# Kernel tuning notes

Hardware: AMD Instinct MI355X
Metric: run time of the kernel (lower is better)

Reference implementation:

```python
import jax, jax.numpy as jnp
import numpy as np

IN_F = 2048
OUT_F = 2048
N_ROWS = 8192


def _perm(n):
    # t_o(n) is a permutation matrix P with P[i, p(i)] = 1, p(i) = (4i mod n) + (4i // n)
    i = np.arange(n)
    return (4 * i) % n + (4 * i) // n


def _inv(p):
    inv = np.empty_like(p)
    inv[p] = np.arange(len(p))
    return inv

# (P_in^T @ H)[a, :] = H[i, :] where p_in(i) = a  ->  rows indexed by inv(p_in)
_INV_P_IN = _inv(_perm(IN_F))
# (H @ P_out)[:, b] = H[:, j] where p_out(j) = b  ->  cols indexed by inv(p_out)
_INV_P_OUT = _inv(_perm(OUT_F))


def make_quaternion_mul(kernel):
    # kernel: (in//4, out); split along dim 1 into quaternion components
    r, i, j, k = jnp.split(kernel, 4, axis=1)
    r2 = jnp.concatenate([r, -i, -j, -k], axis=1)
    i2 = jnp.concatenate([i, r, -k, j], axis=1)
    j2 = jnp.concatenate([j, k, r, -i], axis=1)
    k2 = jnp.concatenate([k, -j, i, r], axis=1)
    return jnp.concatenate([r2, i2, j2, k2], axis=0)  # (in, out)


def setup_inputs() -> dict:
    key = jax.random.key(0)
    k1, k2, k3 = jax.random.split(key, 3)
    inp = jax.random.normal(k1, (N_ROWS, IN_F), dtype=jnp.float32)
    weight = jax.random.normal(k2, (IN_F // 4, OUT_F), dtype=jnp.float32) * (1.0 / np.sqrt(IN_F // 4))
    bias = jax.random.normal(k3, (OUT_F,), dtype=jnp.float32) * 0.01
    return {"input": inp, "weight": weight, "bias": bias}


def reference(input, weight, bias):
    hamilton = make_quaternion_mul(weight)                 # (in, out)
    # swap=True: hamilton = L^T @ hamilton @ R, both pure permutations
    hamilton = hamilton[_INV_P_IN][:, _INV_P_OUT]
    support = input @ hamilton + bias[None, :]             # (N, out)
    return support
```

## Files before the change

### kernel.cpp

```cpp
#include <hip/hip_runtime.h>
#include <stdint.h>

#define IN_F 2048
#define OUT_F 2048
#define N_ROWS 8192

#define BM 256
#define BN 256
#define BK 32
#define NT (IN_F / BK)
#define TM_TILES (N_ROWS / BM)
#define TN_TILES (OUT_F / BN)
#define NWG (TM_TILES * TN_TILES)
#define TILE_SHORTS (BM * BK)
#define BUF_SHORTS (2 * TILE_SHORTS)

typedef __bf16 bf16x8 __attribute__((ext_vector_type(8)));
typedef float f32x4 __attribute__((ext_vector_type(4)));
typedef unsigned short ushortx8 __attribute__((ext_vector_type(8)));

__device__ __forceinline__ unsigned short f2bf(float f) {
  unsigned u = __builtin_bit_cast(unsigned, f);
  u += 0x7FFFu + ((u >> 16) & 1u);
  return (unsigned short)(u >> 16);
}

__device__ __forceinline__ void async16(void* lds, const void* g) {
  __builtin_amdgcn_global_load_lds(
      (const __attribute__((address_space(1))) void*)(uintptr_t)g,
      (__attribute__((address_space(3))) void*)(uint32_t)(uintptr_t)lds,
      16, 0, 0);
}

__device__ __forceinline__ bf16x8 ld8(const unsigned short* p) {
  return __builtin_bit_cast(bf16x8, *reinterpret_cast<const ushortx8*>(p));
}

__global__ __launch_bounds__(256) void k_prep(const float* __restrict__ A,
                                              unsigned short* __restrict__ AbT,
                                              const float* __restrict__ W,
                                              unsigned short* __restrict__ BtT) {
  const int bid = blockIdx.x;
  if (bid < 8192) {
    const int tile = bid >> 2;
    const int t = ((bid & 3) << 8) + threadIdx.x;
    const int r = t >> 2;
    const int ga = (t & 3) ^ ((r >> 1) & 3);
    const int R = tile >> 6, T = tile & 63;
    const float* src = A + (size_t)(R * 256 + r) * IN_F + T * 32 + ga * 8;
    const float4 v0 = *reinterpret_cast<const float4*>(src);
    const float4 v1 = *reinterpret_cast<const float4*>(src + 4);
    ushortx8 o;
    o[0] = f2bf(v0.x); o[1] = f2bf(v0.y); o[2] = f2bf(v0.z); o[3] = f2bf(v0.w);
    o[4] = f2bf(v1.x); o[5] = f2bf(v1.y); o[6] = f2bf(v1.z); o[7] = f2bf(v1.w);
    *reinterpret_cast<ushortx8*>(AbT + (size_t)tile * 8192 + t * 8) = o;
  } else {
    const int bb = bid - 8192;
    const int tile = bb >> 2;
    const int t = ((bb & 3) << 8) + threadIdx.x;
    const int r = t >> 2;
    const int ga = (t & 3) ^ ((r >> 1) & 3);
    const int Ct = tile >> 6, T = tile & 63;
    const int b = Ct * 256 + r;
    const int c = b & 3, v = b >> 2;
    const int a0 = T * 32 + ga * 8;
    ushortx8 o;
#pragma unroll
    for (int e = 0; e < 8; ++e) {
      const int a = a0 + e;
      const int q = a & 3, u = a >> 2;
      float w = W[(size_t)u * OUT_F + ((q ^ c) << 9) + v];
      if ((0x284E >> ((q << 2) | c)) & 1) w = -w;
      o[e] = f2bf(w);
    }
    *reinterpret_cast<ushortx8*>(BtT + (size_t)tile * 8192 + t * 8) = o;
  }
}

__global__ __launch_bounds__(512, 2) void k_gemm(const unsigned short* __restrict__ AbT,
                                                 const unsigned short* __restrict__ BtT,
                                                 const float* __restrict__ bias,
                                                 float* __restrict__ C) {
  __shared__ __align__(16) unsigned short lds[4 * BUF_SHORTS];

  const int tid = threadIdx.x;
  const int lane = tid & 63;
  const int w = tid >> 6;
  const int wm = w >> 2;
  const int wn = w & 3;
  const int fr = lane & 15;
  const int g = lane >> 4;

  const int wg = blockIdx.x;
  const int swz = (wg & 7) * (NWG >> 3) + (wg >> 3);
  const int tm = swz >> 3;
  const int tn = swz & 7;
  const int row0 = tm * BM, col0 = tn * BN;

  const unsigned short* baseA = AbT + (size_t)tm * 64 * 8192;
  const unsigned short* baseB = BtT + (size_t)tn * 64 * 8192;
  const int tOff0 = (w * 128 + lane) * 8;
  const int tOff1 = (w * 128 + 64 + lane) * 8;

#define STAGE(T)                                                   \
  do {                                                             \
    unsigned short* base_ = &lds[((T) & 3) * BUF_SHORTS];          \
    const unsigned short* sa_ = baseA + (size_t)(T) * 8192;        \
    const unsigned short* sb_ = baseB + (size_t)(T) * 8192;        \
    async16(base_ + tOff0, sa_ + tOff0);                           \
    async16(base_ + tOff1, sa_ + tOff1);                           \
    async16(base_ + TILE_SHORTS + tOff0, sb_ + tOff0);             \
    async16(base_ + TILE_SHORTS + tOff1, sb_ + tOff1);             \
  } while (0)

  int offA[8], offB[4];
#pragma unroll
  for (int m = 0; m < 8; ++m) {
    const int r = wm * 128 + m * 16 + fr;
    offA[m] = r * BK + ((g ^ ((r >> 1) & 3)) << 3);
  }
#pragma unroll
  for (int n = 0; n < 4; ++n) {
    const int r = wn * 64 + n * 16 + fr;
    offB[n] = TILE_SHORTS + r * BK + ((g ^ ((r >> 1) & 3)) << 3);
  }

  f32x4 acc[8][4] = {};

#define MFMA_(a_, b_, c_) __builtin_amdgcn_mfma_f32_16x16x32_bf16(a_, b_, c_, 0, 0, 0)

  STAGE(0);
  STAGE(1);
  STAGE(2);

#define TILE(T, VMSTR, DOSTAGE)                                               \
  do {                                                                        \
    asm volatile("s_waitcnt vmcnt(" VMSTR ")" ::: "memory");                  \
    __builtin_amdgcn_s_barrier();                                             \
    __builtin_amdgcn_sched_barrier(0);                                        \
    const unsigned short* b_ = &lds[((T) & 3) * BUF_SHORTS];                  \
    bf16x8 bg[4], af[8];                                                      \
    _Pragma("unroll") for (int n = 0; n < 4; ++n) bg[n] = ld8(b_ + offB[n]);  \
    _Pragma("unroll") for (int m = 0; m < 8; ++m) af[m] = ld8(b_ + offA[m]);  \
    if (DOSTAGE) STAGE((T) + 3);                                              \
    __builtin_amdgcn_s_setprio(1);                                            \
    _Pragma("unroll") for (int m = 0; m < 8; ++m)                             \
      _Pragma("unroll") for (int n = 0; n < 4; ++n)                           \
        acc[m][n] = MFMA_(af[m], bg[n], acc[m][n]);                           \
    __builtin_amdgcn_s_setprio(0);                                            \
  } while (0)

  for (int t = 0; t < NT - 3; ++t) {
    TILE(t, "8", true);
  }
  TILE(NT - 3, "8", false);
  TILE(NT - 2, "4", false);
  TILE(NT - 1, "0", false);

#undef TILE
#undef STAGE

  const int g4 = g << 2;
  float bv[4];
#pragma unroll
  for (int n = 0; n < 4; ++n) bv[n] = bias[col0 + wn * 64 + n * 16 + fr];
#pragma unroll
  for (int m = 0; m < 8; ++m) {
#pragma unroll
    for (int e = 0; e < 4; ++e) {
      const int row = row0 + wm * 128 + m * 16 + g4 + e;
      float* cp = C + (size_t)row * OUT_F + col0 + wn * 64 + fr;
#pragma unroll
      for (int n = 0; n < 4; ++n) cp[n * 16] = acc[m][n][e] + bv[n];
    }
  }
}

__global__ __launch_bounds__(256) void k_naive(const float* __restrict__ A,
                                               const float* __restrict__ W,
                                               const float* __restrict__ bias,
                                               float* __restrict__ C) {
  const int idx = blockIdx.x * 256 + threadIdx.x;
  const int m = idx >> 11;
  const int b = idx & (OUT_F - 1);
  const int c = b & 3, v = b >> 2;
  float acc = 0.f;
  const float* arow = A + (size_t)m * IN_F;
  for (int a = 0; a < IN_F; ++a) {
    const int q = a & 3, u = a >> 2;
    float h = W[(size_t)u * OUT_F + ((q ^ c) << 9) + v];
    if ((0x284E >> ((q << 2) | c)) & 1) h = -h;
    acc += arow[a] * h;
  }
  C[idx] = acc + bias[b];
}

extern "C" void kernel_launch(void* const* d_in, const int* in_sizes, int n_in,
                              void* d_out, int out_size, void* d_ws, size_t ws_size,
                              hipStream_t stream) {
  (void)in_sizes; (void)n_in; (void)out_size;
  const float* inp  = (const float*)d_in[0];
  const float* w    = (const float*)d_in[1];
  const float* bias = (const float*)d_in[2];
  float* out = (float*)d_out;

  const size_t needA = (size_t)N_ROWS * IN_F * sizeof(unsigned short);
  const size_t needH = (size_t)IN_F * OUT_F * sizeof(unsigned short);
  if (ws_size < needA + needH) {
    k_naive<<<(N_ROWS * OUT_F) / 256, 256, 0, stream>>>(inp, w, bias, out);
    return;
  }

  unsigned short* AbT = (unsigned short*)d_ws;
  unsigned short* BtT = AbT + (size_t)N_ROWS * IN_F;

  k_prep<<<8192 + 2048, 256, 0, stream>>>(inp, AbT, w, BtT);
  k_gemm<<<NWG, 512, 0, stream>>>(AbT, BtT, bias, out);
}
```

Baseline: 86.67 us.

## Fuse input fp32-to-bf16 conversion into GEMM A-tile loading

Removes the separate pass that converted the fp32 input to swizzled bf16 in workspace. The GEMM now loads fp32 A rows directly into registers one tile ahead, converts them, and writes the swizzled bf16 tile to LDS, while B still arrives through async global-to-LDS loads. This drops a full write and re-read of the bf16 copy of A. In exchange each A element is read as fp32 by all 8 column-tile workgroups, so A traffic per workgroup doubles, the loads use more VGPRs, and the pipeline is restructured with register double buffering.

Measured after the change: 87.58 us. Within noise of the previous version (+1.1%).

```diff
diff --git a/kernel.cpp b/kernel.cpp
--- a/kernel.cpp
+++ b/kernel.cpp
@@ -36,48 +36,37 @@
   return __builtin_bit_cast(bf16x8, *reinterpret_cast<const ushortx8*>(p));
 }
 
-__global__ __launch_bounds__(256) void k_prep(const float* __restrict__ A,
-                                              unsigned short* __restrict__ AbT,
-                                              const float* __restrict__ W,
-                                              unsigned short* __restrict__ BtT) {
-  const int bid = blockIdx.x;
-  if (bid < 8192) {
-    const int tile = bid >> 2;
-    const int t = ((bid & 3) << 8) + threadIdx.x;
-    const int r = t >> 2;
-    const int ga = (t & 3) ^ ((r >> 1) & 3);
-    const int R = tile >> 6, T = tile & 63;
-    const float* src = A + (size_t)(R * 256 + r) * IN_F + T * 32 + ga * 8;
-    const float4 v0 = *reinterpret_cast<const float4*>(src);
-    const float4 v1 = *reinterpret_cast<const float4*>(src + 4);
-    ushortx8 o;
-    o[0] = f2bf(v0.x); o[1] = f2bf(v0.y); o[2] = f2bf(v0.z); o[3] = f2bf(v0.w);
-    o[4] = f2bf(v1.x); o[5] = f2bf(v1.y); o[6] = f2bf(v1.z); o[7] = f2bf(v1.w);
-    *reinterpret_cast<ushortx8*>(AbT + (size_t)tile * 8192 + t * 8) = o;
-  } else {
-    const int bb = bid - 8192;
-    const int tile = bb >> 2;
-    const int t = ((bb & 3) << 8) + threadIdx.x;
-    const int r = t >> 2;
-    const int ga = (t & 3) ^ ((r >> 1) & 3);
-    const int Ct = tile >> 6, T = tile & 63;
-    const int b = Ct * 256 + r;
-    const int c = b & 3, v = b >> 2;
-    const int a0 = T * 32 + ga * 8;
-    ushortx8 o;
-#pragma unroll
-    for (int e = 0; e < 8; ++e) {
-      const int a = a0 + e;
-      const int q = a & 3, u = a >> 2;
-      float w = W[(size_t)u * OUT_F + ((q ^ c) << 9) + v];
-      if ((0x284E >> ((q << 2) | c)) & 1) w = -w;
-      o[e] = f2bf(w);
-    }
-    *reinterpret_cast<ushortx8*>(BtT + (size_t)tile * 8192 + t * 8) = o;
-  }
-}
-
-__global__ __launch_bounds__(512, 2) void k_gemm(const unsigned short* __restrict__ AbT,
+__device__ __forceinline__ ushortx8 cvt8(float4 a, float4 b) {
+  bf16x8 v;
+  v[0] = (__bf16)a.x; v[1] = (__bf16)a.y; v[2] = (__bf16)a.z; v[3] = (__bf16)a.w;
+  v[4] = (__bf16)b.x; v[5] = (__bf16)b.y; v[6] = (__bf16)b.z; v[7] = (__bf16)b.w;
+  return __builtin_bit_cast(ushortx8, v);
+}
+
+__global__ __launch_bounds__(256) void k_prepB(const float* __restrict__ W,
+                                               unsigned short* __restrict__ BtT) {
+  const int bb = blockIdx.x;
+  const int tile = bb >> 2;
+  const int t = ((bb & 3) << 8) + threadIdx.x;
+  const int r = t >> 2;
+  const int ga = (t & 3) ^ ((r >> 1) & 3);
+  const int Ct = tile >> 6, T = tile & 63;
+  const int b = Ct * 256 + r;
+  const int c = b & 3, v = b >> 2;
+  const int a0 = T * 32 + ga * 8;
+  ushortx8 o;
+#pragma unroll
+  for (int e = 0; e < 8; ++e) {
+    const int a = a0 + e;
+    const int q = a & 3, u = a >> 2;
+    float w = W[(size_t)u * OUT_F + ((q ^ c) << 9) + v];
+    if ((0x284E >> ((q << 2) | c)) & 1) w = -w;
+    o[e] = f2bf(w);
+  }
+  *reinterpret_cast<ushortx8*>(BtT + (size_t)tile * 8192 + t * 8) = o;
+}
+
+__global__ __launch_bounds__(512, 2) void k_gemm(const float* __restrict__ A,
                                                  const unsigned short* __restrict__ BtT,
                                                  const float* __restrict__ bias,
                                                  float* __restrict__ C) {
@@ -97,20 +86,37 @@
   const int tn = swz & 7;
   const int row0 = tm * BM, col0 = tn * BN;
 
-  const unsigned short* baseA = AbT + (size_t)tm * 64 * 8192;
   const unsigned short* baseB = BtT + (size_t)tn * 64 * 8192;
   const int tOff0 = (w * 128 + lane) * 8;
   const int tOff1 = (w * 128 + 64 + lane) * 8;
 
-#define STAGE(T)                                                   \
-  do {                                                             \
-    unsigned short* base_ = &lds[((T) & 3) * BUF_SHORTS];          \
-    const unsigned short* sa_ = baseA + (size_t)(T) * 8192;        \
-    const unsigned short* sb_ = baseB + (size_t)(T) * 8192;        \
-    async16(base_ + tOff0, sa_ + tOff0);                           \
-    async16(base_ + tOff1, sa_ + tOff1);                           \
-    async16(base_ + TILE_SHORTS + tOff0, sb_ + tOff0);             \
-    async16(base_ + TILE_SHORTS + tOff1, sb_ + tOff1);             \
+#define BSTG(T)                                                        \
+  do {                                                                 \
+    unsigned short* d_ = &lds[((T) & 3) * BUF_SHORTS] + TILE_SHORTS;   \
+    const unsigned short* sb_ = baseB + (size_t)(T) * 8192;            \
+    async16(d_ + tOff0, sb_ + tOff0);                                  \
+    async16(d_ + tOff1, sb_ + tOff1);                                  \
+  } while (0)
+
+  const int ga0 = (tid & 3) ^ ((tid >> 3) & 3);
+  const float* srcA0 = A + (size_t)(row0 + (tid >> 2)) * IN_F + ga0 * 8;
+  const float* srcA1 = srcA0 + (size_t)128 * IN_F;
+
+#define ALOAD(T, S_)                                                   \
+  do {                                                                 \
+    const float* s0_ = srcA0 + (T) * 32;                               \
+    const float* s1_ = srcA1 + (T) * 32;                               \
+    S_[0] = *reinterpret_cast<const float4*>(s0_);                     \
+    S_[1] = *reinterpret_cast<const float4*>(s0_ + 4);                 \
+    S_[2] = *reinterpret_cast<const float4*>(s1_);                     \
+    S_[3] = *reinterpret_cast<const float4*>(s1_ + 4);                 \
+  } while (0)
+
+#define AWRITE(T, S_)                                                         \
+  do {                                                                        \
+    unsigned short* d_ = &lds[((T) & 3) * BUF_SHORTS];                        \
+    *reinterpret_cast<ushortx8*>(d_ + tid * 8) = cvt8(S_[0], S_[1]);          \
+    *reinterpret_cast<ushortx8*>(d_ + (tid + 512) * 8) = cvt8(S_[2], S_[3]);  \
   } while (0)
 
   int offA[8], offB[4];
@@ -126,39 +132,110 @@
   }
 
   f32x4 acc[8][4] = {};
+  float4 aE[4], aO[4];
 
 #define MFMA_(a_, b_, c_) __builtin_amdgcn_mfma_f32_16x16x32_bf16(a_, b_, c_, 0, 0, 0)
-
-  STAGE(0);
-  STAGE(1);
-  STAGE(2);
-
-#define TILE(T, VMSTR, DOSTAGE)                                               \
+#define FENCE_ __builtin_amdgcn_sched_barrier(0)
+#define BAR_ __builtin_amdgcn_s_barrier()
+#define LGKM0_ asm volatile("s_waitcnt lgkmcnt(0)" ::: "memory")
+#define VM2_ asm volatile("s_waitcnt vmcnt(2)" ::: "memory")
+#define VM0_ asm volatile("s_waitcnt vmcnt(0)" ::: "memory")
+
+#define STEP(T, LD_, CV_, DOALOAD, DOSTAGE)                                   \
   do {                                                                        \
-    asm volatile("s_waitcnt vmcnt(" VMSTR ")" ::: "memory");                  \
-    __builtin_amdgcn_s_barrier();                                             \
-    __builtin_amdgcn_sched_barrier(0);                                        \
+    BAR_;                                                                     \
+    FENCE_;                                                                   \
     const unsigned short* b_ = &lds[((T) & 3) * BUF_SHORTS];                  \
     bf16x8 bg[4], af[8];                                                      \
     _Pragma("unroll") for (int n = 0; n < 4; ++n) bg[n] = ld8(b_ + offB[n]);  \
     _Pragma("unroll") for (int m = 0; m < 8; ++m) af[m] = ld8(b_ + offA[m]);  \
-    if (DOSTAGE) STAGE((T) + 3);                                              \
+    FENCE_;                                                                   \
+    if (DOALOAD) ALOAD((T) + 4, LD_);                                         \
+    FENCE_;                                                                   \
+    if (DOSTAGE) {                                                            \
+      AWRITE((T) + 3, CV_);                                                   \
+      BSTG((T) + 3);                                                          \
+    }                                                                         \
+    FENCE_;                                                                   \
     __builtin_amdgcn_s_setprio(1);                                            \
     _Pragma("unroll") for (int m = 0; m < 8; ++m)                             \
       _Pragma("unroll") for (int n = 0; n < 4; ++n)                           \
         acc[m][n] = MFMA_(af[m], bg[n], acc[m][n]);                           \
     __builtin_amdgcn_s_setprio(0);                                            \
-  } while (0)
-
-  for (int t = 0; t < NT - 3; ++t) {
-    TILE(t, "8", true);
-  }
-  TILE(NT - 3, "8", false);
-  TILE(NT - 2, "4", false);
-  TILE(NT - 1, "0", false);
-
-#undef TILE
-#undef STAGE
+    FENCE_;                                                                   \
+  } while (0)
+
+  BSTG(0);
+  BSTG(1);
+  BSTG(2);
+  ALOAD(0, aE); AWRITE(0, aE);
+  ALOAD(1, aE); AWRITE(1, aE);
+  ALOAD(2, aE); AWRITE(2, aE);
+  ALOAD(3, aO);
+  LGKM0_;
+  FENCE_;
+
+#pragma unroll 1
+  for (int t = 0; t < NT - 4; t += 2) {
+    STEP(t, aE, aO, true, true);
+    STEP(t + 1, aO, aE, true, true);
+  }
+  STEP(NT - 4, aE, aO, false, true);
+  {
+    BAR_; FENCE_;
+    const unsigned short* b_ = &lds[((NT - 3) & 3) * BUF_SHORTS];
+    bf16x8 bg[4], af[8];
+#pragma unroll
+    for (int n = 0; n < 4; ++n) bg[n] = ld8(b_ + offB[n]);
+#pragma unroll
+    for (int m = 0; m < 8; ++m) af[m] = ld8(b_ + offA[m]);
+    FENCE_;
+    __builtin_amdgcn_s_setprio(1);
+#pragma unroll
+    for (int m = 0; m < 8; ++m)
+#pragma unroll
+      for (int n = 0; n < 4; ++n) acc[m][n] = MFMA_(af[m], bg[n], acc[m][n]);
+    __builtin_amdgcn_s_setprio(0);
+    FENCE_; VM2_;
+  }
+  {
+    BAR_; FENCE_;
+    const unsigned short* b_ = &lds[((NT - 2) & 3) * BUF_SHORTS];
+    bf16x8 bg[4], af[8];
+#pragma unroll
+    for (int n = 0; n < 4; ++n) bg[n] = ld8(b_ + offB[n]);
+#pragma unroll
+    for (int m = 0; m < 8; ++m) af[m] = ld8(b_ + offA[m]);
+    FENCE_;
+    __builtin_amdgcn_s_setprio(1);
+#pragma unroll
+    for (int m = 0; m < 8; ++m)
+#pragma unroll
+      for (int n = 0; n < 4; ++n) acc[m][n] = MFMA_(af[m], bg[n], acc[m][n]);
+    __builtin_amdgcn_s_setprio(0);
+    FENCE_; VM0_;
+  }
+  {
+    BAR_; FENCE_;
+    const unsigned short* b_ = &lds[((NT - 1) & 3) * BUF_SHORTS];
+    bf16x8 bg[4], af[8];
+#pragma unroll
+    for (int n = 0; n < 4; ++n) bg[n] = ld8(b_ + offB[n]);
+#pragma unroll
+    for (int m = 0; m < 8; ++m) af[m] = ld8(b_ + offA[m]);
+    FENCE_;
+    __builtin_amdgcn_s_setprio(1);
+#pragma unroll
+    for (int m = 0; m < 8; ++m)
+#pragma unroll
+      for (int n = 0; n < 4; ++n) acc[m][n] = MFMA_(af[m], bg[n], acc[m][n]);
+    __builtin_amdgcn_s_setprio(0);
+  }
+
+#undef STEP
+#undef BSTG
+#undef ALOAD
+#undef AWRITE
 
   const int g4 = g << 2;
   float bv[4];
@@ -204,16 +281,14 @@
   const float* bias = (const float*)d_in[2];
   float* out = (float*)d_out;
 
-  const size_t needA = (size_t)N_ROWS * IN_F * sizeof(unsigned short);
-  const size_t needH = (size_t)IN_F * OUT_F * sizeof(unsigned short);
-  if (ws_size < needA + needH) {
+  const size_t needB = (size_t)IN_F * OUT_F * sizeof(unsigned short);
+  if (ws_size < needB) {
     k_naive<<<(N_ROWS * OUT_F) / 256, 256, 0, stream>>>(inp, w, bias, out);
     return;
   }
 
-  unsigned short* AbT = (unsigned short*)d_ws;
-  unsigned short* BtT = AbT + (size_t)N_ROWS * IN_F;
-
-  k_prep<<<8192 + 2048, 256, 0, stream>>>(inp, AbT, w, BtT);
-  k_gemm<<<NWG, 512, 0, stream>>>(AbT, BtT, bias, out);
-}
+  unsigned short* BtT = (unsigned short*)d_ws;
+
+  k_prepB<<<2048, 256, 0, stream>>>(w, BtT);
+  k_gemm<<<NWG, 512, 0, stream>>>(inp, BtT, bias, out);
+}
```

## Load B fragments directly from global into registers, stage only A in LDS

Applied to the files above, without the earlier changes.

The GEMM now stages only the A tile through LDS with async global-to-LDS loads. Each wave reads its B fragments straight from global memory into registers, double-buffered one tile ahead, so the prep kernel writes B without the XOR swizzle. This halves LDS footprint and LDS traffic per tile and drops the LDS reads for B. The cost is redundant global/L2 reads of B, since the two wm waves sharing a column slice each load it, plus more register pressure and tighter vmcnt accounting.

Result: slower. 94.83 us (+9.4%).

```diff
diff --git a/kernel.cpp b/kernel.cpp
--- a/kernel.cpp
+++ b/kernel.cpp
@@ -13,7 +13,6 @@
 #define TN_TILES (OUT_F / BN)
 #define NWG (TM_TILES * TN_TILES)
 #define TILE_SHORTS (BM * BK)
-#define BUF_SHORTS (2 * TILE_SHORTS)
 
 typedef __bf16 bf16x8 __attribute__((ext_vector_type(8)));
 typedef float f32x4 __attribute__((ext_vector_type(4)));
@@ -58,12 +57,11 @@
     const int bb = bid - 8192;
     const int tile = bb >> 2;
     const int t = ((bb & 3) << 8) + threadIdx.x;
-    const int r = t >> 2;
-    const int ga = (t & 3) ^ ((r >> 1) & 3);
+    const int r = t >> 2, s = t & 3;
     const int Ct = tile >> 6, T = tile & 63;
     const int b = Ct * 256 + r;
     const int c = b & 3, v = b >> 2;
-    const int a0 = T * 32 + ga * 8;
+    const int a0 = T * 32 + s * 8;
     ushortx8 o;
 #pragma unroll
     for (int e = 0; e < 8; ++e) {
@@ -81,7 +79,7 @@
                                                  const unsigned short* __restrict__ BtT,
                                                  const float* __restrict__ bias,
                                                  float* __restrict__ C) {
-  __shared__ __align__(16) unsigned short lds[4 * BUF_SHORTS];
+  __shared__ __align__(16) unsigned short lds[4 * TILE_SHORTS];
 
   const int tid = threadIdx.x;
   const int lane = tid & 63;
@@ -98,67 +96,83 @@
   const int row0 = tm * BM, col0 = tn * BN;
 
   const unsigned short* baseA = AbT + (size_t)tm * 64 * 8192;
-  const unsigned short* baseB = BtT + (size_t)tn * 64 * 8192;
   const int tOff0 = (w * 128 + lane) * 8;
-  const int tOff1 = (w * 128 + 64 + lane) * 8;
-
-#define STAGE(T)                                                   \
+  const int tOff1 = tOff0 + 512;
+
+#define ASTG(T)                                                    \
   do {                                                             \
-    unsigned short* base_ = &lds[((T) & 3) * BUF_SHORTS];          \
-    const unsigned short* sa_ = baseA + (size_t)(T) * 8192;        \
-    const unsigned short* sb_ = baseB + (size_t)(T) * 8192;        \
-    async16(base_ + tOff0, sa_ + tOff0);                           \
-    async16(base_ + tOff1, sa_ + tOff1);                           \
-    async16(base_ + TILE_SHORTS + tOff0, sb_ + tOff0);             \
-    async16(base_ + TILE_SHORTS + tOff1, sb_ + tOff1);             \
+    unsigned short* d_ = &lds[((T) & 3) * TILE_SHORTS];            \
+    const unsigned short* s_ = baseA + (size_t)(T) * 8192;         \
+    async16(d_ + tOff0, s_ + tOff0);                               \
+    async16(d_ + tOff1, s_ + tOff1);                               \
   } while (0)
 
-  int offA[8], offB[4];
+  const unsigned short* bp[4];
+#pragma unroll
+  for (int n = 0; n < 4; ++n) {
+    const int r = wn * 64 + n * 16 + fr;
+    bp[n] = BtT + (size_t)tn * 64 * 8192 + r * 32 + g * 8;
+  }
+
+  int offA[8];
 #pragma unroll
   for (int m = 0; m < 8; ++m) {
     const int r = wm * 128 + m * 16 + fr;
     offA[m] = r * BK + ((g ^ ((r >> 1) & 3)) << 3);
   }
-#pragma unroll
-  for (int n = 0; n < 4; ++n) {
-    const int r = wn * 64 + n * 16 + fr;
-    offB[n] = TILE_SHORTS + r * BK + ((g ^ ((r >> 1) & 3)) << 3);
-  }
 
   f32x4 acc[8][4] = {};
+  bf16x8 bgE[4], bgO[4];
 
 #define MFMA_(a_, b_, c_) __builtin_amdgcn_mfma_f32_16x16x32_bf16(a_, b_, c_, 0, 0, 0)
-
-  STAGE(0);
-  STAGE(1);
-  STAGE(2);
-
-#define TILE(T, VMSTR, DOSTAGE)                                               \
+#define FENCE_ __builtin_amdgcn_sched_barrier(0)
+
+#define STEP(T, BGC, BGN, DOB, DOA, VMSTR)                                    \
   do {                                                                        \
+    __builtin_amdgcn_s_barrier();                                             \
+    FENCE_;                                                                   \
+    const unsigned short* a_ = &lds[((T) & 3) * TILE_SHORTS];                 \
+    bf16x8 af[8];                                                             \
+    _Pragma("unroll") for (int m = 0; m < 8; ++m) af[m] = ld8(a_ + offA[m]);  \
+    FENCE_;                                                                   \
+    if (DOB) {                                                                \
+      _Pragma("unroll") for (int n = 0; n < 4; ++n)                           \
+        BGN[n] = ld8(bp[n] + (size_t)((T) + 1) * 8192);                       \
+    }                                                                         \
+    FENCE_;                                                                   \
+    if (DOA) ASTG((T) + 3);                                                   \
+    FENCE_;                                                                   \
     asm volatile("s_waitcnt vmcnt(" VMSTR ")" ::: "memory");                  \
-    __builtin_amdgcn_s_barrier();                                             \
-    __builtin_amdgcn_sched_barrier(0);                                        \
-    const unsigned short* b_ = &lds[((T) & 3) * BUF_SHORTS];                  \
-    bf16x8 bg[4], af[8];                                                      \
-    _Pragma("unroll") for (int n = 0; n < 4; ++n) bg[n] = ld8(b_ + offB[n]);  \
-    _Pragma("unroll") for (int m = 0; m < 8; ++m) af[m] = ld8(b_ + offA[m]);  \
-    if (DOSTAGE) STAGE((T) + 3);                                              \
     __builtin_amdgcn_s_setprio(1);                                            \
     _Pragma("unroll") for (int m = 0; m < 8; ++m)                             \
       _Pragma("unroll") for (int n = 0; n < 4; ++n)                           \
-        acc[m][n] = MFMA_(af[m], bg[n], acc[m][n]);                           \
+        acc[m][n] = MFMA_(af[m], BGC[n], acc[m][n]);                          \
     __builtin_amdgcn_s_setprio(0);                                            \
+    FENCE_;                                                                   \
   } while (0)
 
-  for (int t = 0; t < NT - 3; ++t) {
-    TILE(t, "8", true);
-  }
-  TILE(NT - 3, "8", false);
-  TILE(NT - 2, "4", false);
-  TILE(NT - 1, "0", false);
-
-#undef TILE
-#undef STAGE
+  ASTG(0);
+  FENCE_;
+#pragma unroll
+  for (int n = 0; n < 4; ++n) bgE[n] = ld8(bp[n]);
+  FENCE_;
+  ASTG(1);
+  ASTG(2);
+  FENCE_;
+  asm volatile("s_waitcnt vmcnt(8)" ::: "memory");
+
+#pragma unroll 1
+  for (int t = 0; t < NT - 4; t += 2) {
+    STEP(t, bgE, bgO, 1, 1, "8");
+    STEP(t + 1, bgO, bgE, 1, 1, "8");
+  }
+  STEP(NT - 4, bgE, bgO, 1, 1, "8");
+  STEP(NT - 3, bgO, bgE, 1, 0, "6");
+  STEP(NT - 2, bgE, bgO, 1, 0, "4");
+  STEP(NT - 1, bgO, bgE, 0, 0, "0");
+
+#undef STEP
+#undef ASTG
 
   const int g4 = g << 2;
   float bv[4];
@@ -205,8 +219,8 @@
   float* out = (float*)d_out;
 
   const size_t needA = (size_t)N_ROWS * IN_F * sizeof(unsigned short);
-  const size_t needH = (size_t)IN_F * OUT_F * sizeof(unsigned short);
-  if (ws_size < needA + needH) {
+  const size_t needB = (size_t)IN_F * OUT_F * sizeof(unsigned short);
+  if (ws_size < needA + needB) {
     k_naive<<<(N_ROWS * OUT_F) / 256, 256, 0, stream>>>(inp, w, bias, out);
     return;
   }
```
